# Optimization experiments

Hardware: AMD Instinct MI355X
Metric: run time of the kernel (lower is better)

The kernel has to match this reference:

```python
import jax, jax.numpy as jnp
import numpy as np

N_NODES = 100000
N_MOTIFS = 1000000
R_DIM = 1
D_DIM = 64
N_GRAPHS = 128


def setup_inputs() -> dict:
    key = jax.random.key(0)
    ks = jax.random.split(key, 8)
    Q3 = jax.random.normal(ks[0], (N_NODES, R_DIM, D_DIM), dtype=jnp.float32)
    K3 = jax.random.normal(ks[1], (N_NODES, R_DIM, D_DIM), dtype=jnp.float32)
    T_tau_selected = jax.random.normal(ks[2], (N_MOTIFS, R_DIM, D_DIM), dtype=jnp.float32)
    c_3 = jax.random.randint(ks[3], (N_MOTIFS,), 0, N_NODES, dtype=jnp.int32)
    u_3 = jax.random.randint(ks[4], (N_MOTIFS,), 0, N_NODES, dtype=jnp.int32)
    v_3 = jax.random.randint(ks[5], (N_MOTIFS,), 0, N_NODES, dtype=jnp.int32)
    batch = jnp.sort(jax.random.randint(ks[6], (N_NODES,), 0, N_GRAPHS, dtype=jnp.int32))
    lambda_3 = jnp.ones((1,), dtype=jnp.float32)
    beta_3 = jnp.ones((1,), dtype=jnp.float32)
    return {
        "Q3": Q3, "K3": K3, "T_tau_selected": T_tau_selected,
        "lambda_3": lambda_3, "beta_3": beta_3,
        "c_3": c_3, "u_3": u_3, "v_3": v_3, "batch": batch,
        "num_nodes": N_NODES, "num_graphs": N_GRAPHS,
    }


def reference(Q3, K3, T_tau_selected, lambda_3, beta_3, c_3, u_3, v_3, batch, num_nodes, num_graphs):
    R, d = Q3.shape[-2], Q3.shape[-1]
    scale = float((R * d) ** 0.5)
    lam = lambda_3[0]
    beta = beta_3[0]
    # gather triplet embeddings: [M, R, d]
    q = Q3[c_3]
    ku = K3[u_3]
    kv = K3[v_3]
    # fused motif dot: ell[m] = sum_{r,d} q * (ku*kv + T) / sqrt(R*d)
    ell = jnp.sum(q * (ku * kv + T_tau_selected), axis=(-2, -1)) / scale  # [M]
    bell = beta * ell
    # two-pass segment logsumexp per center node (empty nodes -> 0, as in chunked path)
    seg_max = jax.ops.segment_max(bell, c_3, num_segments=num_nodes)  # identity fill for empty
    max_safe = jnp.where(jnp.isfinite(seg_max), seg_max, 0.0)
    sum_exp = jax.ops.segment_sum(jnp.exp(bell - max_safe[c_3]), c_3, num_segments=num_nodes)
    nonempty = sum_exp > 0
    safe_sum = jnp.where(nonempty, sum_exp, 1.0)
    lse = jnp.where(nonempty, jnp.log(safe_sum) + max_safe, 0.0)  # [N]
    # scatter-add node lse to per-graph energy
    graph_lse = jax.ops.segment_sum(lse, batch, num_segments=num_graphs)  # [G]
    return lam / beta * graph_lse
```

## Files before the change

kernel.cpp:

```cpp
#include <hip/hip_runtime.h>
#include <math.h>


typedef float    f32x4 __attribute__((ext_vector_type(4)));
typedef float    f32x2 __attribute__((ext_vector_type(2)));
typedef unsigned u32x2 __attribute__((ext_vector_type(2)));

__global__ void zero_kernel(float* __restrict__ node_sum, int N,
                            float* __restrict__ out, int G) {
    int i = blockIdx.x * blockDim.x + threadIdx.x;
    if (i < N) node_sum[i] = 0.0f;
    if (i < G) out[i] = 0.0f;
}

__global__ __launch_bounds__(256) void prep_kernel(
    const f32x4* __restrict__ Q4, const f32x4* __restrict__ K4,
    u32x2* __restrict__ Qf, u32x2* __restrict__ Kf, int n8)
{
    int i = blockIdx.x * blockDim.x + threadIdx.x;
    if (i >= n8) return;
    f32x4 a = __builtin_nontemporal_load(&Q4[2 * i]);
    f32x4 b = __builtin_nontemporal_load(&Q4[2 * i + 1]);
    u32x2 w;
    int lo = __builtin_amdgcn_cvt_pk_fp8_f32(a.x, a.y, 0, false);
    lo     = __builtin_amdgcn_cvt_pk_fp8_f32(a.z, a.w, lo, true);
    int hi = __builtin_amdgcn_cvt_pk_fp8_f32(b.x, b.y, 0, false);
    hi     = __builtin_amdgcn_cvt_pk_fp8_f32(b.z, b.w, hi, true);
    w.x = (unsigned)lo; w.y = (unsigned)hi;
    Qf[i] = w;

    a = __builtin_nontemporal_load(&K4[2 * i]);
    b = __builtin_nontemporal_load(&K4[2 * i + 1]);
    lo = __builtin_amdgcn_cvt_pk_fp8_f32(a.x, a.y, 0, false);
    lo = __builtin_amdgcn_cvt_pk_fp8_f32(a.z, a.w, lo, true);
    hi = __builtin_amdgcn_cvt_pk_fp8_f32(b.x, b.y, 0, false);
    hi = __builtin_amdgcn_cvt_pk_fp8_f32(b.z, b.w, hi, true);
    w.x = (unsigned)lo; w.y = (unsigned)hi;
    Kf[i] = w;
}

__global__ __launch_bounds__(256) void motif_kernel(
    const unsigned* __restrict__ Qf, const unsigned* __restrict__ Kf,
    const f32x4* __restrict__ T4, const float* __restrict__ beta_p,
    const int* __restrict__ c3, const int* __restrict__ u3,
    const int* __restrict__ v3, float* __restrict__ node_sum,
    int M, float inv_scale)
{
    long long tid = (long long)blockIdx.x * 256 + threadIdx.x;
    int m = (int)(tid >> 3);
    int g = (int)(tid & 7);
    if (m >= M) return;

    int c = c3[m];
    int u = u3[m];
    int v = v3[m];

    const f32x4* tp = T4 + (size_t)m * 16 + g;
    f32x4 t0 = __builtin_nontemporal_load(tp);
    f32x4 t1 = __builtin_nontemporal_load(tp + 8);

    unsigned qw0  = Qf[(size_t)c * 16 + g];
    unsigned qw1  = Qf[(size_t)c * 16 + 8 + g];
    unsigned kuw0 = Kf[(size_t)u * 16 + g];
    unsigned kuw1 = Kf[(size_t)u * 16 + 8 + g];
    unsigned kvw0 = Kf[(size_t)v * 16 + g];
    unsigned kvw1 = Kf[(size_t)v * 16 + 8 + g];

    f32x2 q01  = __builtin_amdgcn_cvt_pk_f32_fp8((int)qw0,  false);
    f32x2 q23  = __builtin_amdgcn_cvt_pk_f32_fp8((int)qw0,  true);
    f32x2 q45  = __builtin_amdgcn_cvt_pk_f32_fp8((int)qw1,  false);
    f32x2 q67  = __builtin_amdgcn_cvt_pk_f32_fp8((int)qw1,  true);
    f32x2 ku01 = __builtin_amdgcn_cvt_pk_f32_fp8((int)kuw0, false);
    f32x2 ku23 = __builtin_amdgcn_cvt_pk_f32_fp8((int)kuw0, true);
    f32x2 ku45 = __builtin_amdgcn_cvt_pk_f32_fp8((int)kuw1, false);
    f32x2 ku67 = __builtin_amdgcn_cvt_pk_f32_fp8((int)kuw1, true);
    f32x2 kv01 = __builtin_amdgcn_cvt_pk_f32_fp8((int)kvw0, false);
    f32x2 kv23 = __builtin_amdgcn_cvt_pk_f32_fp8((int)kvw0, true);
    f32x2 kv45 = __builtin_amdgcn_cvt_pk_f32_fp8((int)kvw1, false);
    f32x2 kv67 = __builtin_amdgcn_cvt_pk_f32_fp8((int)kvw1, true);

    float p =
        q01.x * fmaf(ku01.x, kv01.x, t0.x)
      + q01.y * fmaf(ku01.y, kv01.y, t0.y)
      + q23.x * fmaf(ku23.x, kv23.x, t0.z)
      + q23.y * fmaf(ku23.y, kv23.y, t0.w)
      + q45.x * fmaf(ku45.x, kv45.x, t1.x)
      + q45.y * fmaf(ku45.y, kv45.y, t1.y)
      + q67.x * fmaf(ku67.x, kv67.x, t1.z)
      + q67.y * fmaf(ku67.y, kv67.y, t1.w);

    #pragma unroll
    for (int off = 4; off > 0; off >>= 1)
        p += __shfl_xor(p, off);

    if (g == 0) {
        float bell = beta_p[0] * p * inv_scale;
        atomicAdd(&node_sum[c], __expf(bell));
    }
}

__global__ __launch_bounds__(256) void node_kernel(
    const float* __restrict__ node_sum, const int* __restrict__ batch,
    const float* __restrict__ lam_p, const float* __restrict__ beta_p,
    float* __restrict__ out, int N, int G)
{
    extern __shared__ float gacc[];
    for (int j = threadIdx.x; j < G; j += blockDim.x) gacc[j] = 0.0f;
    __syncthreads();

    int i = blockIdx.x * blockDim.x + threadIdx.x;
    if (i < N) {
        float s = node_sum[i];
        if (s > 0.0f) {
            atomicAdd(&gacc[batch[i]], logf(s));
        }
    }
    __syncthreads();

    float coef = lam_p[0] / beta_p[0];
    for (int j = threadIdx.x; j < G; j += blockDim.x) {
        float v = gacc[j];
        if (v != 0.0f) atomicAdd(&out[j], coef * v);
    }
}

extern "C" void kernel_launch(void* const* d_in, const int* in_sizes, int n_in,
                              void* d_out, int out_size, void* d_ws, size_t ws_size,
                              hipStream_t stream) {
    const float* Q    = (const float*)d_in[0];
    const float* K    = (const float*)d_in[1];
    const float* T    = (const float*)d_in[2];
    const float* lam  = (const float*)d_in[3];
    const float* beta = (const float*)d_in[4];
    const int* c3     = (const int*)d_in[5];
    const int* u3     = (const int*)d_in[6];
    const int* v3     = (const int*)d_in[7];
    const int* batch  = (const int*)d_in[8];

    const int M = in_sizes[5];
    const int N = in_sizes[8];
    const int G = out_size;
    const int RD = in_sizes[0] / N;
    const int n8 = in_sizes[0] / 8;
    const float inv_scale = 1.0f / sqrtf((float)RD);

    float* node_sum = (float*)d_ws;
    size_t off = (((size_t)N * sizeof(float)) + 1023) & ~(size_t)1023;
    unsigned* Qf = (unsigned*)((char*)d_ws + off);
    unsigned* Kf = Qf + (size_t)n8 * 2;
    float* out = (float*)d_out;

    int zmax = (N > G) ? N : G;
    zero_kernel<<<(zmax + 255) / 256, 256, 0, stream>>>(node_sum, N, out, G);

    prep_kernel<<<(n8 + 255) / 256, 256, 0, stream>>>(
        (const f32x4*)Q, (const f32x4*)K, (u32x2*)Qf, (u32x2*)Kf, n8);

    long long total_threads = (long long)M * 8;
    int mgrid = (int)((total_threads + 255) / 256);
    motif_kernel<<<mgrid, 256, 0, stream>>>(
        Qf, Kf, (const f32x4*)T, beta, c3, u3, v3, node_sum, M, inv_scale);

    node_kernel<<<(N + 255) / 256, 256, G * sizeof(float), stream>>>(
        node_sum, batch, lam, beta, out, N, G);
}
```

Baseline: 108.5 us.

## Use grid-stride persistent motif kernel with prefetched next indices

The motif kernel now runs a fixed grid of 2048 blocks. Each 8-lane group loops over motifs with a grid stride instead of handling exactly one motif. Inside the loop it loads the next motif's c/u/v indices before doing the current motif's arithmetic, so the index-load latency overlaps with compute. This cuts block launch overhead and hides part of the dependent-gather latency, at the cost of fewer waves in flight, which may reduce memory-level parallelism.

```diff
diff --git a/kernel.cpp b/kernel.cpp
--- a/kernel.cpp
+++ b/kernel.cpp
@@ -44,58 +44,67 @@
     const f32x4* __restrict__ T4, const float* __restrict__ beta_p,
     const int* __restrict__ c3, const int* __restrict__ u3,
     const int* __restrict__ v3, float* __restrict__ node_sum,
-    int M, float inv_scale)
+    int M, float inv_scale, int nGroups)
 {
-    long long tid = (long long)blockIdx.x * 256 + threadIdx.x;
-    int m = (int)(tid >> 3);
-    int g = (int)(tid & 7);
-    if (m >= M) return;
+    int tid = blockIdx.x * 256 + threadIdx.x;
+    int grp = tid >> 3;
+    int g = tid & 7;
+    if (grp >= M) return;
 
-    int c = c3[m];
-    int u = u3[m];
-    int v = v3[m];
+    const float beta_scale = beta_p[0] * inv_scale;
 
-    const f32x4* tp = T4 + (size_t)m * 16 + g;
-    f32x4 t0 = __builtin_nontemporal_load(tp);
-    f32x4 t1 = __builtin_nontemporal_load(tp + 8);
+    int m = grp;
+    int c = c3[m], u = u3[m], v = v3[m];
 
-    unsigned qw0  = Qf[(size_t)c * 16 + g];
-    unsigned qw1  = Qf[(size_t)c * 16 + 8 + g];
-    unsigned kuw0 = Kf[(size_t)u * 16 + g];
-    unsigned kuw1 = Kf[(size_t)u * 16 + 8 + g];
-    unsigned kvw0 = Kf[(size_t)v * 16 + g];
-    unsigned kvw1 = Kf[(size_t)v * 16 + 8 + g];
+    while (true) {
+        const f32x4* tp = T4 + (size_t)m * 16 + g;
+        f32x4 t0 = __builtin_nontemporal_load(tp);
+        f32x4 t1 = __builtin_nontemporal_load(tp + 8);
+        unsigned qw0  = Qf[(size_t)c * 16 + g];
+        unsigned qw1  = Qf[(size_t)c * 16 + 8 + g];
+        unsigned kuw0 = Kf[(size_t)u * 16 + g];
+        unsigned kuw1 = Kf[(size_t)u * 16 + 8 + g];
+        unsigned kvw0 = Kf[(size_t)v * 16 + g];
+        unsigned kvw1 = Kf[(size_t)v * 16 + 8 + g];
 
-    f32x2 q01  = __builtin_amdgcn_cvt_pk_f32_fp8((int)qw0,  false);
-    f32x2 q23  = __builtin_amdgcn_cvt_pk_f32_fp8((int)qw0,  true);
-    f32x2 q45  = __builtin_amdgcn_cvt_pk_f32_fp8((int)qw1,  false);
-    f32x2 q67  = __builtin_amdgcn_cvt_pk_f32_fp8((int)qw1,  true);
-    f32x2 ku01 = __builtin_amdgcn_cvt_pk_f32_fp8((int)kuw0, false);
-    f32x2 ku23 = __builtin_amdgcn_cvt_pk_f32_fp8((int)kuw0, true);
-    f32x2 ku45 = __builtin_amdgcn_cvt_pk_f32_fp8((int)kuw1, false);
-    f32x2 ku67 = __builtin_amdgcn_cvt_pk_f32_fp8((int)kuw1, true);
-    f32x2 kv01 = __builtin_amdgcn_cvt_pk_f32_fp8((int)kvw0, false);
-    f32x2 kv23 = __builtin_amdgcn_cvt_pk_f32_fp8((int)kvw0, true);
-    f32x2 kv45 = __builtin_amdgcn_cvt_pk_f32_fp8((int)kvw1, false);
-    f32x2 kv67 = __builtin_amdgcn_cvt_pk_f32_fp8((int)kvw1, true);
+        int m_next = m + nGroups;
+        bool has_next = (m_next < M);
+        int cn = 0, un = 0, vn = 0;
+        if (has_next) { cn = c3[m_next]; un = u3[m_next]; vn = v3[m_next]; }
 
-    float p =
-        q01.x * fmaf(ku01.x, kv01.x, t0.x)
-      + q01.y * fmaf(ku01.y, kv01.y, t0.y)
-      + q23.x * fmaf(ku23.x, kv23.x, t0.z)
-      + q23.y * fmaf(ku23.y, kv23.y, t0.w)
-      + q45.x * fmaf(ku45.x, kv45.x, t1.x)
-      + q45.y * fmaf(ku45.y, kv45.y, t1.y)
-      + q67.x * fmaf(ku67.x, kv67.x, t1.z)
-      + q67.y * fmaf(ku67.y, kv67.y, t1.w);
+        f32x2 q01  = __builtin_amdgcn_cvt_pk_f32_fp8((int)qw0,  false);
+        f32x2 q23  = __builtin_amdgcn_cvt_pk_f32_fp8((int)qw0,  true);
+        f32x2 q45  = __builtin_amdgcn_cvt_pk_f32_fp8((int)qw1,  false);
+        f32x2 q67  = __builtin_amdgcn_cvt_pk_f32_fp8((int)qw1,  true);
+        f32x2 ku01 = __builtin_amdgcn_cvt_pk_f32_fp8((int)kuw0, false);
+        f32x2 ku23 = __builtin_amdgcn_cvt_pk_f32_fp8((int)kuw0, true);
+        f32x2 ku45 = __builtin_amdgcn_cvt_pk_f32_fp8((int)kuw1, false);
+        f32x2 ku67 = __builtin_amdgcn_cvt_pk_f32_fp8((int)kuw1, true);
+        f32x2 kv01 = __builtin_amdgcn_cvt_pk_f32_fp8((int)kvw0, false);
+        f32x2 kv23 = __builtin_amdgcn_cvt_pk_f32_fp8((int)kvw0, true);
+        f32x2 kv45 = __builtin_amdgcn_cvt_pk_f32_fp8((int)kvw1, false);
+        f32x2 kv67 = __builtin_amdgcn_cvt_pk_f32_fp8((int)kvw1, true);
 
-    #pragma unroll
-    for (int off = 4; off > 0; off >>= 1)
-        p += __shfl_xor(p, off);
+        float p =
+            q01.x * fmaf(ku01.x, kv01.x, t0.x)
+          + q01.y * fmaf(ku01.y, kv01.y, t0.y)
+          + q23.x * fmaf(ku23.x, kv23.x, t0.z)
+          + q23.y * fmaf(ku23.y, kv23.y, t0.w)
+          + q45.x * fmaf(ku45.x, kv45.x, t1.x)
+          + q45.y * fmaf(ku45.y, kv45.y, t1.y)
+          + q67.x * fmaf(ku67.x, kv67.x, t1.z)
+          + q67.y * fmaf(ku67.y, kv67.y, t1.w);
 
-    if (g == 0) {
-        float bell = beta_p[0] * p * inv_scale;
-        atomicAdd(&node_sum[c], __expf(bell));
+        #pragma unroll
+        for (int off = 4; off > 0; off >>= 1)
+            p += __shfl_xor(p, off);
+
+        if (g == 0) {
+            atomicAdd(&node_sum[c], __expf(beta_scale * p));
+        }
+
+        if (!has_next) break;
+        m = m_next; c = cn; u = un; v = vn;
     }
 }
 
@@ -156,10 +165,11 @@
     prep_kernel<<<(n8 + 255) / 256, 256, 0, stream>>>(
         (const f32x4*)Q, (const f32x4*)K, (u32x2*)Qf, (u32x2*)Kf, n8);
 
-    long long total_threads = (long long)M * 8;
-    int mgrid = (int)((total_threads + 255) / 256);
-    motif_kernel<<<mgrid, 256, 0, stream>>>(
-        Qf, Kf, (const f32x4*)T, beta, c3, u3, v3, node_sum, M, inv_scale);
+    const int mblocks = 2048;
+    const int nGroups = mblocks * 256 / 8;
+    motif_kernel<<<mblocks, 256, 0, stream>>>(
+        Qf, Kf, (const f32x4*)T, beta, c3, u3, v3, node_sum,
+        M, inv_scale, nGroups);
 
     node_kernel<<<(N + 255) / 256, 256, G * sizeof(float), stream>>>(
         node_sum, batch, lam, beta, out, N, G);
```

Measured after the change: 114.0 us. +5.1%, slower.
